# Kernel optimization log

Hardware: AMD Instinct MI355X
Metric: run time of the kernel (lower is better)

## Reference

```python
import jax, jax.numpy as jnp
import numpy as np

N = 192    # num_nodes == number of trees
M = 256    # max_node_number (feature width per tree level)
D = 1024   # tree depth (NATree.shape[1])
K = M - N + 1  # Conv2 kernel size


def setup_inputs() -> dict:
    key = jax.random.key(0)
    k1, k2, k3, k4, k5, k6 = jax.random.split(key, 6)
    s = 0.05
    NATree = jax.random.normal(k1, (N, D, M), jnp.float32)
    W = jax.random.normal(k2, (M, M, 2), jnp.float32) * s   # Conv1d weight [out, in, kernel=2]
    b = jax.random.normal(k3, (M,), jnp.float32) * s        # Conv1d bias
    x = jax.random.normal(k4, (N, M), jnp.float32) * s      # self.x parameter
    W2 = jax.random.normal(k5, (K,), jnp.float32) * s       # Conv2 weight (out=1,in=1,kernel=K)
    b2 = jax.random.normal(k6, (), jnp.float32) * s         # Conv2 bias
    return {"NATree": NATree, "W": W, "b": b, "x": x, "W2": W2, "b2": b2}


def reference(NATree, W, b, x, W2, b2):
    # Conv1d(k=2) on cat([row_j, h]) splits into two MxM matmuls:
    #   h_new = W0 @ row_j + W1 @ h + b + sigmoid(row_j)
    W0 = W[:, :, 0]  # multiplies row_j (first position in concat)
    W1 = W[:, :, 1]  # multiplies carried state h
    rows = NATree[:, :-1, :]  # [N, D-1, M], levels j = 0 .. D-2
    # Precompute the per-level additive term in one batched matmul.
    u = jnp.einsum('ndm,km->ndk', rows, W0) + b + jax.nn.sigmoid(rows)  # [N, D-1, M]
    h0 = NATree[:, -1, :]  # [N, M], initial state = last tree level
    # Walk levels j = D-2 down to 0.
    u_seq = jnp.flip(u, axis=1).transpose(1, 0, 2)  # [D-1, N, M]

    def step(h, u_j):
        return u_j + h @ W1.T, None

    h_fin, _ = jax.lax.scan(step, h0, u_seq)  # [N, M]
    res = jax.nn.relu(h_fin + x)  # [N, M]
    # Conv2: 1-ch cross-correlation, kernel K, output length M-K+1 = N.
    out = jax.lax.conv_general_dilated(
        res[:, None, :], W2[None, None, :], window_strides=(1,), padding='VALID') + b2
    return jax.nn.sigmoid(out[:, 0, :])  # [N, N]
```

## Files before the change

### kernel.cpp

```cpp
#include <hip/hip_runtime.h>
#include <hip/hip_bf16.h>
#include <cstddef>

#define DN 192
#define DM 256
#define DD 1024
#define DK 65
#define OUTW 192

using f32x4 = __attribute__((ext_vector_type(4))) float;
using s16x8 = __attribute__((ext_vector_type(8))) short;

__device__ __forceinline__ float sigm(float v) { return 1.0f / (1.0f + __expf(-v)); }
__device__ __forceinline__ unsigned short f2b(float f) {
    __hip_bfloat16 h = __float2bfloat16(f);
    return *reinterpret_cast<unsigned short*>(&h);
}
__device__ __forceinline__ float b2f(unsigned short s) {
    __hip_bfloat16 h = *reinterpret_cast<__hip_bfloat16*>(&s);
    return __bfloat162float(h);
}

#define OFF_QF   0u
#define OFF_A2   65536u
#define OFF_A4   131072u
#define OFF_A8   196608u
#define OFF_A16  262144u
#define OFF_A32  327680u
#define OFF_A64  393216u
#define OFF_QB   458752u
#define OFF_W0B  491520u
#define OFF_P8B  524288u
#define OFF_P64B 557056u
#define OFF_SA1  589824u
#define OFF_SA2  3735552u
#define OFF_VC   4521984u
#define TIER_A_BYTES 118751232ULL
#define TIER_B_BYTES  30670848ULL

__global__ __launch_bounds__(256) void k_prep2(const float* __restrict__ W,
                                               float* __restrict__ ws) {
    const int bid = blockIdx.x, t = threadIdx.x;
    if (bid < 256) {
        const int c = bid, m = t;
        ws[OFF_QF + m * 256 + c] = W[(size_t)(c * 256 + m) * 2 + 1];
    } else {
        const int which = (bid - 256) >> 5;
        const int e = ((bid - 256) & 31) * 256 + t;
        const int ct = e >> 9, ks = (e >> 6) & 7, l = e & 63;
        const int c = ct * 16 + (l & 15);
        const int mb = ks * 32 + (l >> 4) * 8;
        s16x8 pk;
#pragma unroll
        for (int j = 0; j < 8; ++j)
            pk[j] = (short)f2b(W[(size_t)(c * 256 + mb + j) * 2 + (which ? 0 : 1)]);
        float* dst = ws + (which ? OFF_W0B : OFF_QB);
        reinterpret_cast<s16x8*>(dst)[e] = pk;
    }
}

__global__ __launch_bounds__(256) void k_sq256(const float* __restrict__ A,
                                               float* __restrict__ C,
                                               ushort* __restrict__ bfrag) {
    __shared__ float ar[256];
    const int r0 = blockIdx.x, k = threadIdx.x;
    ar[k] = A[r0 * 256 + k];
    __syncthreads();
    float a0 = 0.f, a1 = 0.f, a2 = 0.f, a3 = 0.f;
    for (int m = 0; m < 256; m += 8) {
        a0 += ar[m + 0] * A[(m + 0) * 256 + k] + ar[m + 4] * A[(m + 4) * 256 + k];
        a1 += ar[m + 1] * A[(m + 1) * 256 + k] + ar[m + 5] * A[(m + 5) * 256 + k];
        a2 += ar[m + 2] * A[(m + 2) * 256 + k] + ar[m + 6] * A[(m + 6) * 256 + k];
        a3 += ar[m + 3] * A[(m + 3) * 256 + k] + ar[m + 7] * A[(m + 7) * 256 + k];
    }
    const float v = (a0 + a1) + (a2 + a3);
    C[r0 * 256 + k] = v;
    if (bfrag) {
        const int entry = ((k >> 4) * 8 + (r0 >> 5)) * 64 + ((r0 >> 3) & 3) * 16 + (k & 15);
        bfrag[entry * 8 + (r0 & 7)] = f2b(v);
    }
}

__global__ __launch_bounds__(512) void k_phase1a(const float* __restrict__ NAT,
                                                 const float* __restrict__ bvec,
                                                 const float* __restrict__ ws,
                                                 unsigned short* __restrict__ Vc,
                                                 int d0_base) {
    __shared__ short Rl[4][8][65][8];
    const int rt = blockIdx.x;
    const int dq = blockIdx.y;
    const int n0 = rt * 16;
    const int tid = threadIdx.x;
    const int w = tid >> 6, l = tid & 63;
    const ushort* W0b = reinterpret_cast<const ushort*>(ws + OFF_W0B);

    {
        const int r = (tid >> 3) & 15, dd = tid >> 7, ks = tid & 7;
        const int dg = d0_base + dq * 4 + dd;
        const float* src = NAT + ((size_t)(n0 + r) * DD + dg) * DM + ks * 32;
        float f[32];
#pragma unroll
        for (int q = 0; q < 8; ++q) {
            const float4 v4 = *reinterpret_cast<const float4*>(src + q * 4);
            f[q * 4 + 0] = v4.x; f[q * 4 + 1] = v4.y; f[q * 4 + 2] = v4.z; f[q * 4 + 3] = v4.w;
        }
#pragma unroll
        for (int g = 0; g < 4; ++g) {
            s16x8 pk;
#pragma unroll
            for (int j = 0; j < 8; ++j) pk[j] = (short)f2b(f[g * 8 + j]);
            *reinterpret_cast<s16x8*>(&Rl[dd][ks][r + 16 * g][0]) = pk;
        }
    }
    __syncthreads();

    f32x4 acc[4][2];
    float bcol[2];
#pragma unroll
    for (int c = 0; c < 2; ++c) bcol[c] = bvec[w * 32 + c * 16 + (l & 15)];
#pragma unroll
    for (int dd = 0; dd < 4; ++dd)
#pragma unroll
        for (int c = 0; c < 2; ++c) {
            const int col = w * 32 + c * 16 + (l & 15);
            const int ksm = col >> 5, sl = 16 * ((col >> 3) & 3), jb = col & 7;
#pragma unroll
            for (int r = 0; r < 4; ++r) {
                const int row15 = (l >> 4) * 4 + r;
                unsigned short sv = (unsigned short)Rl[dd][ksm][row15 + sl][jb];
                acc[dd][c][r] = bcol[c] + sigm(b2f(sv));
            }
        }

    for (int ks = 0; ks < 8; ++ks) {
        const s16x8 gb0 = *reinterpret_cast<const s16x8*>(W0b + (((2 * w + 0) * 8 + ks) * 64 + l) * 8);
        const s16x8 gb1 = *reinterpret_cast<const s16x8*>(W0b + (((2 * w + 1) * 8 + ks) * 64 + l) * 8);
#pragma unroll
        for (int dd = 0; dd < 4; ++dd) {
            const s16x8 a = *reinterpret_cast<const s16x8*>(&Rl[dd][ks][l][0]);
            acc[dd][0] = __builtin_amdgcn_mfma_f32_16x16x32_bf16(a, gb0, acc[dd][0], 0, 0, 0);
            acc[dd][1] = __builtin_amdgcn_mfma_f32_16x16x32_bf16(a, gb1, acc[dd][1], 0, 0, 0);
        }
    }

#pragma unroll
    for (int dd = 0; dd < 4; ++dd)
#pragma unroll
        for (int c = 0; c < 2; ++c) {
            const size_t base = ((((size_t)(dq * 4 + dd) * 12 + rt) * 16 + (2 * w + c)) * 64 + l);
            ushort4 o;
            o.x = f2b(acc[dd][c][0]); o.y = f2b(acc[dd][c][1]);
            o.z = f2b(acc[dd][c][2]); o.w = f2b(acc[dd][c][3]);
            reinterpret_cast<ushort4*>(Vc)[base] = o;
        }
}

__global__ __launch_bounds__(512) void k_scan(const void* __restrict__ Vin, int in_bf16,
                                              const float* __restrict__ NAT, int grp_base,
                                              const float* __restrict__ ws, unsigned qb_off,
                                              int nsteps,
                                              void* __restrict__ OutC, int out_bf16,
                                              const float* __restrict__ xin,
                                              const float* __restrict__ W2,
                                              const float* __restrict__ b2p,
                                              float* __restrict__ outF) {
    __shared__ __align__(16) char smem[33856];
    short (*Sl)[2][8][64][8] = reinterpret_cast<short (*)[2][8][64][8]>(smem);
    float (*resl)[260]       = reinterpret_cast<float (*)[260]>(smem);
    float* w2l               = reinterpret_cast<float*>(smem + 33280);
    const int rt2 = blockIdx.x;
    const int grp = blockIdx.y;
    const int tid = threadIdx.x;
    const int w = tid >> 6, l = tid & 63;
    const ushort* Qb = reinterpret_cast<const ushort*>(ws + qb_off);

    s16x8 qreg[2][8];
#pragma unroll
    for (int c = 0; c < 2; ++c)
#pragma unroll
        for (int ks = 0; ks < 8; ++ks)
            qreg[c][ks] = *reinterpret_cast<const s16x8*>(Qb + (((2 * w + c) * 8 + ks) * 64 + l) * 8);

    f32x4 acc[2][2];
    int cur = 0;
    for (int it = 0; it < nsteps; ++it) {
        const int d = grp * nsteps + (nsteps - 1) - it;
        if (it == 0 && NAT != nullptr && (grp_base + grp) == 127) {
#pragma unroll
            for (int rt = 0; rt < 2; ++rt)
#pragma unroll
                for (int c = 0; c < 2; ++c) {
                    const int col = w * 32 + c * 16 + (l & 15);
#pragma unroll
                    for (int r = 0; r < 4; ++r) {
                        const int n = rt2 * 32 + rt * 16 + (l >> 4) * 4 + r;
                        acc[rt][c][r] = NAT[((size_t)n * DD + (DD - 1)) * DM + col];
                    }
                }
        } else {
#pragma unroll
            for (int rt = 0; rt < 2; ++rt)
#pragma unroll
                for (int c = 0; c < 2; ++c) {
                    const size_t base = (((size_t)d * 12 + (rt2 * 2 + rt)) * 16 + (2 * w + c)) * 64 + l;
                    if (in_bf16) {
                        const ushort4 v = reinterpret_cast<const ushort4*>(Vin)[base];
                        acc[rt][c][0] = b2f(v.x); acc[rt][c][1] = b2f(v.y);
                        acc[rt][c][2] = b2f(v.z); acc[rt][c][3] = b2f(v.w);
                    } else {
                        acc[rt][c] = reinterpret_cast<const f32x4*>(Vin)[base];
                    }
                }
        }
        if (it > 0) {
#pragma unroll
            for (int ks = 0; ks < 8; ++ks) {
                const s16x8 a0 = *reinterpret_cast<const s16x8*>(&Sl[cur][0][ks][l][0]);
                const s16x8 a1 = *reinterpret_cast<const s16x8*>(&Sl[cur][1][ks][l][0]);
                acc[0][0] = __builtin_amdgcn_mfma_f32_16x16x32_bf16(a0, qreg[0][ks], acc[0][0], 0, 0, 0);
                acc[0][1] = __builtin_amdgcn_mfma_f32_16x16x32_bf16(a0, qreg[1][ks], acc[0][1], 0, 0, 0);
                acc[1][0] = __builtin_amdgcn_mfma_f32_16x16x32_bf16(a1, qreg[0][ks], acc[1][0], 0, 0, 0);
                acc[1][1] = __builtin_amdgcn_mfma_f32_16x16x32_bf16(a1, qreg[1][ks], acc[1][1], 0, 0, 0);
            }
        }
        if (it < nsteps - 1) {
#pragma unroll
            for (int rt = 0; rt < 2; ++rt)
#pragma unroll
                for (int c = 0; c < 2; ++c) {
                    const int col = w * 32 + c * 16 + (l & 15);
                    const int sl = 16 * ((col >> 3) & 3), jb = col & 7;
#pragma unroll
                    for (int r = 0; r < 4; ++r) {
                        const int row15 = (l >> 4) * 4 + r;
                        Sl[cur ^ 1][rt][w][row15 + sl][jb] = (short)f2b(acc[rt][c][r]);
                    }
                }
            __syncthreads();
            cur ^= 1;
        }
    }

    if (outF == nullptr) {
        const int gg = grp_base + grp;
#pragma unroll
        for (int rt = 0; rt < 2; ++rt)
#pragma unroll
            for (int c = 0; c < 2; ++c) {
                const size_t base = (((size_t)gg * 12 + (rt2 * 2 + rt)) * 16 + (2 * w + c)) * 64 + l;
                if (out_bf16) {
                    ushort4 o;
                    o.x = f2b(acc[rt][c][0]); o.y = f2b(acc[rt][c][1]);
                    o.z = f2b(acc[rt][c][2]); o.w = f2b(acc[rt][c][3]);
                    reinterpret_cast<ushort4*>(OutC)[base] = o;
                } else {
                    reinterpret_cast<f32x4*>(OutC)[base] = acc[rt][c];
                }
            }
    } else {
        if (tid < DK) w2l[tid] = W2[tid];
        __syncthreads();
#pragma unroll
        for (int rt = 0; rt < 2; ++rt)
#pragma unroll
            for (int c = 0; c < 2; ++c) {
                const int col = w * 32 + c * 16 + (l & 15);
#pragma unroll
                for (int r = 0; r < 4; ++r) {
                    const int row = rt * 16 + (l >> 4) * 4 + r;
                    const int n = rt2 * 32 + row;
                    const float v = acc[rt][c][r] + xin[(size_t)n * DM + col];
                    resl[row][col] = v > 0.f ? v : 0.f;
                }
            }
        __syncthreads();
        const float b2v = *b2p;
        const int k = tid & 255;
        for (int rr = tid >> 8; rr < 32; rr += 2) {
            if (k < OUTW) {
                float o = b2v;
#pragma unroll
                for (int i = 0; i < DK; ++i) o += resl[rr][k + i] * w2l[i];
                outF[(size_t)(rt2 * 32 + rr) * OUTW + k] = sigm(o);
            }
        }
    }
}

#define OCB 16
#define ONB 64
#define OR1 24
#define ORB1 8
#define OPSTR 260
#define O_W0T 0u
#define O_W1T 65536u
#define O_PW  131072u
#define O_S   (131072u + 5u*65536u)

__global__ __launch_bounds__(256) void k_prep_o(const float* __restrict__ W, float* __restrict__ ws) {
    const int m = blockIdx.x, k = threadIdx.x;
    const float2 w = *reinterpret_cast<const float2*>(W + (size_t)k * 512 + m * 2);
    ws[O_W0T + m * 256 + k] = w.x;
    ws[O_W1T + m * 256 + k] = w.y;
}

__global__ __launch_bounds__(256) void k_sq_o(const float* __restrict__ A, float* __restrict__ C) {
    __shared__ float ar[4][OPSTR];
    const int r0 = blockIdx.x * 4, k = threadIdx.x;
    for (int r = 0; r < 4; ++r) ar[r][k] = A[(r0 + r) * 256 + k];
    __syncthreads();
    float a0 = 0.f, a1 = 0.f, a2 = 0.f, a3 = 0.f;
    for (int m = 0; m < 256; m += 4) {
        const float p0 = A[(m + 0) * 256 + k], p1 = A[(m + 1) * 256 + k];
        const float p2 = A[(m + 2) * 256 + k], p3 = A[(m + 3) * 256 + k];
        float4 t;
        t = *reinterpret_cast<const float4*>(&ar[0][m]); a0 += t.x * p0 + t.y * p1 + t.z * p2 + t.w * p3;
        t = *reinterpret_cast<const float4*>(&ar[1][m]); a1 += t.x * p0 + t.y * p1 + t.z * p2 + t.w * p3;
        t = *reinterpret_cast<const float4*>(&ar[2][m]); a2 += t.x * p0 + t.y * p1 + t.z * p2 + t.w * p3;
        t = *reinterpret_cast<const float4*>(&ar[3][m]); a3 += t.x * p0 + t.y * p1 + t.z * p2 + t.w * p3;
    }
    C[(r0 + 0) * 256 + k] = a0; C[(r0 + 1) * 256 + k] = a1;
    C[(r0 + 2) * 256 + k] = a2; C[(r0 + 3) * 256 + k] = a3;
}

__global__ __launch_bounds__(256) void k_phase1_o(const float* __restrict__ NAT,
                                                  const float* __restrict__ bvec,
                                                  const float* __restrict__ ws,
                                                  float* __restrict__ Sall) {
    __shared__ float Sl[OR1 * OPSTR];
    __shared__ float Rl[OR1 * OPSTR];
    const int rb = blockIdx.x, bb = blockIdx.y, tid = threadIdx.x;
    const int tj = tid & 63, ti = tid >> 6, n0 = rb * OR1;
    const float* __restrict__ W0t = ws + O_W0T;
    const float* __restrict__ W1t = ws + O_W1T;
    const float4 bv = *reinterpret_cast<const float4*>(bvec + 4 * tj);
    float acc[6][4];
    for (int it = 0; it < OCB; ++it) {
        const int d = bb * OCB + (OCB - 1) - it;
#pragma unroll
        for (int q = 0; q < 6; ++q) {
            const int row = q * 4 + ti;
            const float4 v = *reinterpret_cast<const float4*>(NAT + ((size_t)(n0 + row) * DD + d) * DM + 4 * tj);
            *reinterpret_cast<float4*>(&Rl[row * OPSTR + 4 * tj]) = v;
        }
        __syncthreads();
        if (d == DD - 1) {
#pragma unroll
            for (int r = 0; r < 6; ++r) {
                const float4 v = *reinterpret_cast<const float4*>(&Rl[(ti * 6 + r) * OPSTR + 4 * tj]);
                acc[r][0] = v.x; acc[r][1] = v.y; acc[r][2] = v.z; acc[r][3] = v.w;
            }
        } else {
#pragma unroll
            for (int r = 0; r < 6; ++r) {
                const float4 v = *reinterpret_cast<const float4*>(&Rl[(ti * 6 + r) * OPSTR + 4 * tj]);
                acc[r][0] = bv.x + sigm(v.x); acc[r][1] = bv.y + sigm(v.y);
                acc[r][2] = bv.z + sigm(v.z); acc[r][3] = bv.w + sigm(v.w);
            }
            if (it == 0) {
#pragma unroll 2
                for (int m = 0; m < DM; m += 2) {
                    const float4 w0a = *reinterpret_cast<const float4*>(W0t + m * DM + 4 * tj);
                    const float4 w0b = *reinterpret_cast<const float4*>(W0t + (m + 1) * DM + 4 * tj);
#pragma unroll
                    for (int r = 0; r < 6; ++r) {
                        const float2 rv = *reinterpret_cast<const float2*>(&Rl[(ti * 6 + r) * OPSTR + m]);
                        acc[r][0] += rv.x * w0a.x + rv.y * w0b.x;
                        acc[r][1] += rv.x * w0a.y + rv.y * w0b.y;
                        acc[r][2] += rv.x * w0a.z + rv.y * w0b.z;
                        acc[r][3] += rv.x * w0a.w + rv.y * w0b.w;
                    }
                }
            } else {
#pragma unroll 2
                for (int m = 0; m < DM; m += 2) {
                    const float4 w0a = *reinterpret_cast<const float4*>(W0t + m * DM + 4 * tj);
                    const float4 w0b = *reinterpret_cast<const float4*>(W0t + (m + 1) * DM + 4 * tj);
                    const float4 w1a = *reinterpret_cast<const float4*>(W1t + m * DM + 4 * tj);
                    const float4 w1b = *reinterpret_cast<const float4*>(W1t + (m + 1) * DM + 4 * tj);
#pragma unroll
                    for (int r = 0; r < 6; ++r) {
                        const float2 rv = *reinterpret_cast<const float2*>(&Rl[(ti * 6 + r) * OPSTR + m]);
                        const float2 sv = *reinterpret_cast<const float2*>(&Sl[(ti * 6 + r) * OPSTR + m]);
                        acc[r][0] += rv.x * w0a.x + rv.y * w0b.x + sv.x * w1a.x + sv.y * w1b.x;
                        acc[r][1] += rv.x * w0a.y + rv.y * w0b.y + sv.x * w1a.y + sv.y * w1b.y;
                        acc[r][2] += rv.x * w0a.z + rv.y * w0b.z + sv.x * w1a.z + sv.y * w1b.z;
                        acc[r][3] += rv.x * w0a.w + rv.y * w0b.w + sv.x * w1a.w + sv.y * w1b.w;
                    }
                }
            }
        }
        __syncthreads();
#pragma unroll
        for (int r = 0; r < 6; ++r) {
            float4 v; v.x = acc[r][0]; v.y = acc[r][1]; v.z = acc[r][2]; v.w = acc[r][3];
            *reinterpret_cast<float4*>(&Sl[(ti * 6 + r) * OPSTR + 4 * tj]) = v;
        }
        __syncthreads();
    }
    float* dst = Sall + ((size_t)bb * DN + n0) * DM;
#pragma unroll
    for (int r = 0; r < 6; ++r) {
        float4 v; v.x = acc[r][0]; v.y = acc[r][1]; v.z = acc[r][2]; v.w = acc[r][3];
        *reinterpret_cast<float4*>(dst + (size_t)(ti * 6 + r) * DM + 4 * tj) = v;
    }
}

__global__ __launch_bounds__(256) void k_phase2_o(const float* __restrict__ Sall,
                                                  const float* __restrict__ P,
                                                  const float* __restrict__ x,
                                                  const float* __restrict__ W2,
                                                  const float* __restrict__ b2p,
                                                  float* __restrict__ out) {
    __shared__ float Tl[2][DM];
    __shared__ float resl[DM];
    const int n = blockIdx.x, k = threadIdx.x;
    float a = Sall[((size_t)(ONB - 1) * DN + n) * DM + k];
    Tl[0][k] = a;
    __syncthreads();
    int cur = 0;
    for (int b = ONB - 2; b >= 0; --b) {
        const float s0 = Sall[((size_t)b * DN + n) * DM + k];
        float a0 = 0.f, a1 = 0.f, a2 = 0.f, a3 = 0.f;
        for (int m = 0; m < DM; m += 8) {
            const float4 t0 = *reinterpret_cast<const float4*>(&Tl[cur][m]);
            const float4 t1 = *reinterpret_cast<const float4*>(&Tl[cur][m + 4]);
            a0 += t0.x * P[(m + 0) * DM + k] + t1.x * P[(m + 4) * DM + k];
            a1 += t0.y * P[(m + 1) * DM + k] + t1.y * P[(m + 5) * DM + k];
            a2 += t0.z * P[(m + 2) * DM + k] + t1.z * P[(m + 6) * DM + k];
            a3 += t0.w * P[(m + 3) * DM + k] + t1.w * P[(m + 7) * DM + k];
        }
        a = s0 + ((a0 + a1) + (a2 + a3));
        Tl[cur ^ 1][k] = a;
        __syncthreads();
        cur ^= 1;
    }
    const float b2v = *b2p;
    float r = a + x[(size_t)n * DM + k];
    resl[k] = r > 0.f ? r : 0.f;
    __syncthreads();
    if (k < OUTW) {
        float o = b2v;
#pragma unroll 5
        for (int i = 0; i < DK; ++i) o += resl[k + i] * W2[i];
        out[(size_t)n * OUTW + k] = sigm(o);
    }
}

extern "C" void kernel_launch(void* const* d_in, const int* in_sizes, int n_in,
                              void* d_out, int out_size, void* d_ws, size_t ws_size,
                              hipStream_t stream) {
    const float* NAT = (const float*)d_in[0];
    const float* W   = (const float*)d_in[1];
    const float* bv  = (const float*)d_in[2];
    const float* x   = (const float*)d_in[3];
    const float* W2  = (const float*)d_in[4];
    const float* b2  = (const float*)d_in[5];
    float* out = (float*)d_out;
    float* ws  = (float*)d_ws;

    if (ws_size >= TIER_B_BYTES) {
        k_prep2<<<320, 256, 0, stream>>>(W, ws);
        k_sq256<<<256, 256, 0, stream>>>(ws + OFF_QF,  ws + OFF_A2,  nullptr);
        k_sq256<<<256, 256, 0, stream>>>(ws + OFF_A2,  ws + OFF_A4,  nullptr);
        k_sq256<<<256, 256, 0, stream>>>(ws + OFF_A4,  ws + OFF_A8,
                                         reinterpret_cast<ushort*>(ws + OFF_P8B));
        k_sq256<<<256, 256, 0, stream>>>(ws + OFF_A8,  ws + OFF_A16, nullptr);
        k_sq256<<<256, 256, 0, stream>>>(ws + OFF_A16, ws + OFF_A32, nullptr);
        k_sq256<<<256, 256, 0, stream>>>(ws + OFF_A32, ws + OFF_A64,
                                         reinterpret_cast<ushort*>(ws + OFF_P64B));

        unsigned short* Vc = reinterpret_cast<unsigned short*>(ws + OFF_VC);
        float* SA1 = ws + OFF_SA1;
        float* SA2 = ws + OFF_SA2;

        if (ws_size >= TIER_A_BYTES) {
            k_phase1a<<<dim3(12, 256), 512, 0, stream>>>(NAT, bv, ws, Vc, 0);
            k_scan<<<dim3(6, 128), 512, 0, stream>>>(Vc, 1, NAT, 0, ws, OFF_QB, 8,
                                                     SA1, 1, nullptr, nullptr, nullptr, nullptr);
        } else {
            for (int c = 0; c < 8; ++c) {
                k_phase1a<<<dim3(12, 32), 512, 0, stream>>>(NAT, bv, ws, Vc, c * 128);
                k_scan<<<dim3(6, 16), 512, 0, stream>>>(Vc, 1, NAT, c * 16, ws, OFF_QB, 8,
                                                        SA1, 1, nullptr, nullptr, nullptr, nullptr);
            }
        }
        k_scan<<<dim3(6, 16), 512, 0, stream>>>(SA1, 1, nullptr, 0, ws, OFF_P8B, 8,
                                                SA2, 0, nullptr, nullptr, nullptr, nullptr);
        k_scan<<<dim3(6, 1), 512, 0, stream>>>(SA2, 0, nullptr, 0, ws, OFF_P64B, 16,
                                               nullptr, 0, x, W2, b2, out);
    } else {
        k_prep_o<<<256, 256, 0, stream>>>(W, ws);
        const float* q = ws + O_W1T;
        float* pw = ws + O_PW;
        k_sq_o<<<64, 256, 0, stream>>>(q,              pw + 0 * 65536);
        k_sq_o<<<64, 256, 0, stream>>>(pw + 0 * 65536, pw + 1 * 65536);
        k_sq_o<<<64, 256, 0, stream>>>(pw + 1 * 65536, pw + 2 * 65536);
        k_sq_o<<<64, 256, 0, stream>>>(pw + 2 * 65536, pw + 3 * 65536);
        float* Sall = ws + O_S;
        k_phase1_o<<<dim3(ORB1, ONB), 256, 0, stream>>>(NAT, bv, ws, Sall);
        k_phase2_o<<<192, 256, 0, stream>>>(Sall, pw + 3 * 65536, x, W2, b2, out);
    }
}
```

Measured before the change: 456.3 us.

## Fuse W0 projection into first-level scan kernel, dropping the Vc intermediate

Replaces the separate k_phase1a (bf16 projection of NATree rows by W0, plus sigmoid and bias) and the first k_scan pass with one k_fused kernel. For each group of 8 levels it loads rows with register prefetch, computes the u term with MFMA and immediately applies the recurrence. This removes the large bf16 Vc buffer write and re-read through global memory, and with it the tiered workspace logic. It also launches the fused kernel before the power-matrix squaring kernels. The cost is more per-block serial work and register pressure under launch_bounds(512,4), and NATree loading is now interleaved with the sequential steps.

```diff
diff --git a/kernel.cpp b/kernel.cpp
--- a/kernel.cpp
+++ b/kernel.cpp
@@ -34,9 +34,7 @@
 #define OFF_P64B 557056u
 #define OFF_SA1  589824u
 #define OFF_SA2  3735552u
-#define OFF_VC   4521984u
-#define TIER_A_BYTES 118751232ULL
-#define TIER_B_BYTES  30670848ULL
+#define MFMA_NEED_BYTES 18087936ULL
 
 __global__ __launch_bounds__(256) void k_prep2(const float* __restrict__ W,
                                                float* __restrict__ ws) {
@@ -81,82 +79,151 @@
     }
 }
 
-__global__ __launch_bounds__(512) void k_phase1a(const float* __restrict__ NAT,
-                                                 const float* __restrict__ bvec,
-                                                 const float* __restrict__ ws,
-                                                 unsigned short* __restrict__ Vc,
-                                                 int d0_base) {
-    __shared__ short Rl[4][8][65][8];
-    const int rt = blockIdx.x;
-    const int dq = blockIdx.y;
-    const int n0 = rt * 16;
+__global__ __launch_bounds__(512, 4) void k_fused(const float* __restrict__ NAT,
+                                                  const float* __restrict__ bvec,
+                                                  const float* __restrict__ ws,
+                                                  ushort* __restrict__ SA1) {
+    __shared__ short Rl[2][8][66][8];
+    __shared__ short Sl[2][2][8][64][8];
+    const int rt2 = blockIdx.x;
+    const int grp = blockIdx.y;
     const int tid = threadIdx.x;
     const int w = tid >> 6, l = tid & 63;
+    const int n0 = rt2 * 32;
     const ushort* W0b = reinterpret_cast<const ushort*>(ws + OFF_W0B);
-
+    const ushort* Qb  = reinterpret_cast<const ushort*>(ws + OFF_QB);
+
+    s16x8 qreg[2][8];
+#pragma unroll
+    for (int c = 0; c < 2; ++c)
+#pragma unroll
+        for (int ks = 0; ks < 8; ++ks)
+            qreg[c][ks] = *reinterpret_cast<const s16x8*>(Qb + (((2 * w + c) * 8 + ks) * 64 + l) * 8);
+
+    const int srow = tid >> 4;
+    const int sks  = (tid >> 1) & 7;
+    const int shalf = tid & 1;
+    const float* sbase = NAT + (size_t)(n0 + srow) * DD * DM + sks * 32 + shalf * 16;
+
+    float4 rv0, rv1, rv2, rv3;
     {
-        const int r = (tid >> 3) & 15, dd = tid >> 7, ks = tid & 7;
-        const int dg = d0_base + dq * 4 + dd;
-        const float* src = NAT + ((size_t)(n0 + r) * DD + dg) * DM + ks * 32;
-        float f[32];
-#pragma unroll
-        for (int q = 0; q < 8; ++q) {
-            const float4 v4 = *reinterpret_cast<const float4*>(src + q * 4);
-            f[q * 4 + 0] = v4.x; f[q * 4 + 1] = v4.y; f[q * 4 + 2] = v4.z; f[q * 4 + 3] = v4.w;
-        }
-#pragma unroll
-        for (int g = 0; g < 4; ++g) {
-            s16x8 pk;
-#pragma unroll
-            for (int j = 0; j < 8; ++j) pk[j] = (short)f2b(f[g * 8 + j]);
-            *reinterpret_cast<s16x8*>(&Rl[dd][ks][r + 16 * g][0]) = pk;
-        }
-    }
-    __syncthreads();
-
-    f32x4 acc[4][2];
-    float bcol[2];
-#pragma unroll
-    for (int c = 0; c < 2; ++c) bcol[c] = bvec[w * 32 + c * 16 + (l & 15)];
-#pragma unroll
-    for (int dd = 0; dd < 4; ++dd)
+        const float* p = sbase + (size_t)(grp * 8 + 7) * DM;
+        rv0 = *reinterpret_cast<const float4*>(p + 0);
+        rv1 = *reinterpret_cast<const float4*>(p + 4);
+        rv2 = *reinterpret_cast<const float4*>(p + 8);
+        rv3 = *reinterpret_cast<const float4*>(p + 12);
+    }
+    const float bcol0 = bvec[w * 32 + (l & 15)];
+    const float bcol1 = bvec[w * 32 + 16 + (l & 15)];
+
+    f32x4 acc[2][2];
+    int cur = 0;
+    for (int it = 0; it < 8; ++it) {
+        const int d = grp * 8 + 7 - it;
+        {
+            const int g0 = shalf * 2;
+            s16x8 pk0, pk1;
+            pk0[0] = (short)f2b(rv0.x); pk0[1] = (short)f2b(rv0.y);
+            pk0[2] = (short)f2b(rv0.z); pk0[3] = (short)f2b(rv0.w);
+            pk0[4] = (short)f2b(rv1.x); pk0[5] = (short)f2b(rv1.y);
+            pk0[6] = (short)f2b(rv1.z); pk0[7] = (short)f2b(rv1.w);
+            pk1[0] = (short)f2b(rv2.x); pk1[1] = (short)f2b(rv2.y);
+            pk1[2] = (short)f2b(rv2.z); pk1[3] = (short)f2b(rv2.w);
+            pk1[4] = (short)f2b(rv3.x); pk1[5] = (short)f2b(rv3.y);
+            pk1[6] = (short)f2b(rv3.z); pk1[7] = (short)f2b(rv3.w);
+            *reinterpret_cast<s16x8*>(&Rl[srow >> 4][sks][(srow & 15) + 16 * g0][0]) = pk0;
+            *reinterpret_cast<s16x8*>(&Rl[srow >> 4][sks][(srow & 15) + 16 * (g0 + 1)][0]) = pk1;
+        }
+        if (it < 7) {
+            const float* p = sbase + (size_t)(d - 1) * DM;
+            rv0 = *reinterpret_cast<const float4*>(p + 0);
+            rv1 = *reinterpret_cast<const float4*>(p + 4);
+            rv2 = *reinterpret_cast<const float4*>(p + 8);
+            rv3 = *reinterpret_cast<const float4*>(p + 12);
+        }
+        __syncthreads();
+
+        if (grp == 127 && it == 0) {
+#pragma unroll
+            for (int rt = 0; rt < 2; ++rt)
+#pragma unroll
+                for (int c = 0; c < 2; ++c) {
+                    const int col = w * 32 + c * 16 + (l & 15);
+#pragma unroll
+                    for (int r = 0; r < 4; ++r) {
+                        const int n = n0 + rt * 16 + (l >> 4) * 4 + r;
+                        acc[rt][c][r] = NAT[((size_t)n * DD + (DD - 1)) * DM + col];
+                    }
+                }
+        } else {
+#pragma unroll
+            for (int rt = 0; rt < 2; ++rt)
+#pragma unroll
+                for (int c = 0; c < 2; ++c) {
+                    const int col = w * 32 + c * 16 + (l & 15);
+                    const int ksm = col >> 5, sl = 16 * ((col >> 3) & 3), jb = col & 7;
+                    const float bc = c ? bcol1 : bcol0;
+#pragma unroll
+                    for (int r = 0; r < 4; ++r) {
+                        const int row15 = (l >> 4) * 4 + r;
+                        const unsigned short sv = (unsigned short)Rl[rt][ksm][row15 + sl][jb];
+                        acc[rt][c][r] = bc + sigm(b2f(sv));
+                    }
+                }
+#pragma unroll
+            for (int ks = 0; ks < 8; ++ks) {
+                const s16x8 gb0 = *reinterpret_cast<const s16x8*>(W0b + (((2 * w + 0) * 8 + ks) * 64 + l) * 8);
+                const s16x8 gb1 = *reinterpret_cast<const s16x8*>(W0b + (((2 * w + 1) * 8 + ks) * 64 + l) * 8);
+                const s16x8 a0 = *reinterpret_cast<const s16x8*>(&Rl[0][ks][l][0]);
+                const s16x8 a1 = *reinterpret_cast<const s16x8*>(&Rl[1][ks][l][0]);
+                acc[0][0] = __builtin_amdgcn_mfma_f32_16x16x32_bf16(a0, gb0, acc[0][0], 0, 0, 0);
+                acc[0][1] = __builtin_amdgcn_mfma_f32_16x16x32_bf16(a0, gb1, acc[0][1], 0, 0, 0);
+                acc[1][0] = __builtin_amdgcn_mfma_f32_16x16x32_bf16(a1, gb0, acc[1][0], 0, 0, 0);
+                acc[1][1] = __builtin_amdgcn_mfma_f32_16x16x32_bf16(a1, gb1, acc[1][1], 0, 0, 0);
+            }
+        }
+        if (it > 0) {
+#pragma unroll
+            for (int ks = 0; ks < 8; ++ks) {
+                const s16x8 s0 = *reinterpret_cast<const s16x8*>(&Sl[cur][0][ks][l][0]);
+                const s16x8 s1 = *reinterpret_cast<const s16x8*>(&Sl[cur][1][ks][l][0]);
+                acc[0][0] = __builtin_amdgcn_mfma_f32_16x16x32_bf16(s0, qreg[0][ks], acc[0][0], 0, 0, 0);
+                acc[0][1] = __builtin_amdgcn_mfma_f32_16x16x32_bf16(s0, qreg[1][ks], acc[0][1], 0, 0, 0);
+                acc[1][0] = __builtin_amdgcn_mfma_f32_16x16x32_bf16(s1, qreg[0][ks], acc[1][0], 0, 0, 0);
+                acc[1][1] = __builtin_amdgcn_mfma_f32_16x16x32_bf16(s1, qreg[1][ks], acc[1][1], 0, 0, 0);
+            }
+        }
+        if (it < 7) {
+#pragma unroll
+            for (int rt = 0; rt < 2; ++rt)
+#pragma unroll
+                for (int c = 0; c < 2; ++c) {
+                    const int col = w * 32 + c * 16 + (l & 15);
+                    const int sl = 16 * ((col >> 3) & 3), jb = col & 7;
+#pragma unroll
+                    for (int r = 0; r < 4; ++r) {
+                        const int row15 = (l >> 4) * 4 + r;
+                        Sl[cur ^ 1][rt][w][row15 + sl][jb] = (short)f2b(acc[rt][c][r]);
+                    }
+                }
+            __syncthreads();
+            cur ^= 1;
+        }
+    }
+
+#pragma unroll
+    for (int rt = 0; rt < 2; ++rt)
 #pragma unroll
         for (int c = 0; c < 2; ++c) {
-            const int col = w * 32 + c * 16 + (l & 15);
-            const int ksm = col >> 5, sl = 16 * ((col >> 3) & 3), jb = col & 7;
-#pragma unroll
-            for (int r = 0; r < 4; ++r) {
-                const int row15 = (l >> 4) * 4 + r;
-                unsigned short sv = (unsigned short)Rl[dd][ksm][row15 + sl][jb];
-                acc[dd][c][r] = bcol[c] + sigm(b2f(sv));
-            }
-        }
-
-    for (int ks = 0; ks < 8; ++ks) {
-        const s16x8 gb0 = *reinterpret_cast<const s16x8*>(W0b + (((2 * w + 0) * 8 + ks) * 64 + l) * 8);
-        const s16x8 gb1 = *reinterpret_cast<const s16x8*>(W0b + (((2 * w + 1) * 8 + ks) * 64 + l) * 8);
-#pragma unroll
-        for (int dd = 0; dd < 4; ++dd) {
-            const s16x8 a = *reinterpret_cast<const s16x8*>(&Rl[dd][ks][l][0]);
-            acc[dd][0] = __builtin_amdgcn_mfma_f32_16x16x32_bf16(a, gb0, acc[dd][0], 0, 0, 0);
-            acc[dd][1] = __builtin_amdgcn_mfma_f32_16x16x32_bf16(a, gb1, acc[dd][1], 0, 0, 0);
-        }
-    }
-
-#pragma unroll
-    for (int dd = 0; dd < 4; ++dd)
-#pragma unroll
-        for (int c = 0; c < 2; ++c) {
-            const size_t base = ((((size_t)(dq * 4 + dd) * 12 + rt) * 16 + (2 * w + c)) * 64 + l);
+            const size_t base = (((size_t)grp * 12 + (rt2 * 2 + rt)) * 16 + (2 * w + c)) * 64 + l;
             ushort4 o;
-            o.x = f2b(acc[dd][c][0]); o.y = f2b(acc[dd][c][1]);
-            o.z = f2b(acc[dd][c][2]); o.w = f2b(acc[dd][c][3]);
-            reinterpret_cast<ushort4*>(Vc)[base] = o;
+            o.x = f2b(acc[rt][c][0]); o.y = f2b(acc[rt][c][1]);
+            o.z = f2b(acc[rt][c][2]); o.w = f2b(acc[rt][c][3]);
+            reinterpret_cast<ushort4*>(SA1)[base] = o;
         }
 }
 
 __global__ __launch_bounds__(512) void k_scan(const void* __restrict__ Vin, int in_bf16,
-                                              const float* __restrict__ NAT, int grp_base,
                                               const float* __restrict__ ws, unsigned qb_off,
                                               int nsteps,
                                               void* __restrict__ OutC, int out_bf16,
@@ -185,33 +252,19 @@
     int cur = 0;
     for (int it = 0; it < nsteps; ++it) {
         const int d = grp * nsteps + (nsteps - 1) - it;
-        if (it == 0 && NAT != nullptr && (grp_base + grp) == 127) {
-#pragma unroll
-            for (int rt = 0; rt < 2; ++rt)
-#pragma unroll
-                for (int c = 0; c < 2; ++c) {
-                    const int col = w * 32 + c * 16 + (l & 15);
-#pragma unroll
-                    for (int r = 0; r < 4; ++r) {
-                        const int n = rt2 * 32 + rt * 16 + (l >> 4) * 4 + r;
-                        acc[rt][c][r] = NAT[((size_t)n * DD + (DD - 1)) * DM + col];
-                    }
-                }
-        } else {
-#pragma unroll
-            for (int rt = 0; rt < 2; ++rt)
-#pragma unroll
-                for (int c = 0; c < 2; ++c) {
-                    const size_t base = (((size_t)d * 12 + (rt2 * 2 + rt)) * 16 + (2 * w + c)) * 64 + l;
-                    if (in_bf16) {
-                        const ushort4 v = reinterpret_cast<const ushort4*>(Vin)[base];
-                        acc[rt][c][0] = b2f(v.x); acc[rt][c][1] = b2f(v.y);
-                        acc[rt][c][2] = b2f(v.z); acc[rt][c][3] = b2f(v.w);
-                    } else {
-                        acc[rt][c] = reinterpret_cast<const f32x4*>(Vin)[base];
-                    }
-                }
-        }
+#pragma unroll
+        for (int rt = 0; rt < 2; ++rt)
+#pragma unroll
+            for (int c = 0; c < 2; ++c) {
+                const size_t base = (((size_t)d * 12 + (rt2 * 2 + rt)) * 16 + (2 * w + c)) * 64 + l;
+                if (in_bf16) {
+                    const ushort4 v = reinterpret_cast<const ushort4*>(Vin)[base];
+                    acc[rt][c][0] = b2f(v.x); acc[rt][c][1] = b2f(v.y);
+                    acc[rt][c][2] = b2f(v.z); acc[rt][c][3] = b2f(v.w);
+                } else {
+                    acc[rt][c] = reinterpret_cast<const f32x4*>(Vin)[base];
+                }
+            }
         if (it > 0) {
 #pragma unroll
             for (int ks = 0; ks < 8; ++ks) {
@@ -242,12 +295,11 @@
     }
 
     if (outF == nullptr) {
-        const int gg = grp_base + grp;
 #pragma unroll
         for (int rt = 0; rt < 2; ++rt)
 #pragma unroll
             for (int c = 0; c < 2; ++c) {
-                const size_t base = (((size_t)gg * 12 + (rt2 * 2 + rt)) * 16 + (2 * w + c)) * 64 + l;
+                const size_t base = (((size_t)grp * 12 + (rt2 * 2 + rt)) * 16 + (2 * w + c)) * 64 + l;
                 if (out_bf16) {
                     ushort4 o;
                     o.x = f2b(acc[rt][c][0]); o.y = f2b(acc[rt][c][1]);
@@ -459,8 +511,14 @@
     float* out = (float*)d_out;
     float* ws  = (float*)d_ws;
 
-    if (ws_size >= TIER_B_BYTES) {
+    if (ws_size >= MFMA_NEED_BYTES) {
         k_prep2<<<320, 256, 0, stream>>>(W, ws);
+
+        ushort* SA1 = reinterpret_cast<ushort*>(ws + OFF_SA1);
+        float*  SA2 = ws + OFF_SA2;
+
+        k_fused<<<dim3(6, 128), 512, 0, stream>>>(NAT, bv, ws, SA1);
+
         k_sq256<<<256, 256, 0, stream>>>(ws + OFF_QF,  ws + OFF_A2,  nullptr);
         k_sq256<<<256, 256, 0, stream>>>(ws + OFF_A2,  ws + OFF_A4,  nullptr);
         k_sq256<<<256, 256, 0, stream>>>(ws + OFF_A4,  ws + OFF_A8,
@@ -470,24 +528,9 @@
         k_sq256<<<256, 256, 0, stream>>>(ws + OFF_A32, ws + OFF_A64,
                                          reinterpret_cast<ushort*>(ws + OFF_P64B));
 
-        unsigned short* Vc = reinterpret_cast<unsigned short*>(ws + OFF_VC);
-        float* SA1 = ws + OFF_SA1;
-        float* SA2 = ws + OFF_SA2;
-
-        if (ws_size >= TIER_A_BYTES) {
-            k_phase1a<<<dim3(12, 256), 512, 0, stream>>>(NAT, bv, ws, Vc, 0);
-            k_scan<<<dim3(6, 128), 512, 0, stream>>>(Vc, 1, NAT, 0, ws, OFF_QB, 8,
-                                                     SA1, 1, nullptr, nullptr, nullptr, nullptr);
-        } else {
-            for (int c = 0; c < 8; ++c) {
-                k_phase1a<<<dim3(12, 32), 512, 0, stream>>>(NAT, bv, ws, Vc, c * 128);
-                k_scan<<<dim3(6, 16), 512, 0, stream>>>(Vc, 1, NAT, c * 16, ws, OFF_QB, 8,
-                                                        SA1, 1, nullptr, nullptr, nullptr, nullptr);
-            }
-        }
-        k_scan<<<dim3(6, 16), 512, 0, stream>>>(SA1, 1, nullptr, 0, ws, OFF_P8B, 8,
+        k_scan<<<dim3(6, 16), 512, 0, stream>>>(SA1, 1, ws, OFF_P8B, 8,
                                                 SA2, 0, nullptr, nullptr, nullptr, nullptr);
-        k_scan<<<dim3(6, 1), 512, 0, stream>>>(SA2, 0, nullptr, 0, ws, OFF_P64B, 16,
+        k_scan<<<dim3(6, 1), 512, 0, stream>>>(SA2, 0, ws, OFF_P64B, 16,
                                                nullptr, 0, x, W2, b2, out);
     } else {
         k_prep_o<<<256, 256, 0, stream>>>(W, ws);
```

Result: slower. 513.8 us (+12.6%).
